# Kernel optimization log

Measured on AMD Instinct MI355X. Metric: run time of the kernel, lower is better.

## Reference

```python
import jax, jax.numpy as jnp
import numpy as np

N_NODES = 100000
N_EDGES = 1200000
D_IN = 64
D_HID = 64
D_OUT = 64


def setup_inputs() -> dict:
    key = jax.random.key(0)
    k1, k2, k3, k4, k5, k6 = jax.random.split(key, 6)
    x = jax.random.normal(k1, (N_NODES, D_IN), dtype=jnp.float32)
    edge_index = jax.random.randint(k2, (2, N_EDGES), 0, N_NODES, dtype=jnp.int32)
    s1 = 1.0 / np.sqrt(2 * D_IN)
    s2 = 1.0 / np.sqrt(2 * D_HID)
    W1 = jax.random.uniform(k3, (2 * D_IN, D_HID), jnp.float32, -s1, s1)
    b1 = jax.random.uniform(k4, (D_HID,), jnp.float32, -s1, s1)
    W2 = jax.random.uniform(k5, (2 * D_HID, D_OUT), jnp.float32, -s2, s2)
    b2 = jax.random.uniform(k6, (D_OUT,), jnp.float32, -s2, s2)
    return {"x": x, "edge_index": edge_index, "W1": W1, "b1": b1, "W2": W2, "b2": b2}


def _sage_conv(x, row, col, W, b):
    n = x.shape[0]
    # gather neighbor features and scatter-sum to destinations
    neighbor_sum = jax.ops.segment_sum(x[col], row, num_segments=n)  # [N, d]
    deg = jax.ops.segment_sum(jnp.ones(row.shape[0], x.dtype), row, num_segments=n)
    deg = jnp.maximum(deg, 1.0)
    neighbor_agg = neighbor_sum / deg[:, None]
    out = jnp.concatenate([x, neighbor_agg], axis=-1)  # [N, 2d]
    return out @ W + b


def reference(x, edge_index, W1, b1, W2, b2):
    row, col = edge_index[0], edge_index[1]
    h = jax.nn.relu(_sage_conv(x, row, col, W1, b1))
    # dropout is identity at inference (training=False)
    return _sage_conv(h, row, col, W2, b2)
```

## Files before the change

### kernel.cpp

```cpp
#include <hip/hip_runtime.h>

#define N_NODES 100000
#define N_EDGES 1200000
#define D 64

#define BSHIFT 8
#define NB ((N_NODES + 255) >> BSHIFT)
#define EPB 2048
#define P1_BLOCKS ((N_EDGES + EPB - 1) / EPB)
#define P2_CAP 4096

typedef short bf16x8 __attribute__((ext_vector_type(8)));
typedef float f32x4 __attribute__((ext_vector_type(4)));
typedef unsigned short u16x4 __attribute__((ext_vector_type(4)));
typedef unsigned short u16x8 __attribute__((ext_vector_type(8)));

__device__ __forceinline__ short f2bf(float x) {
  unsigned u = __float_as_uint(x);
  unsigned r = (u + 0x7FFFu + ((u >> 16) & 1u)) >> 16;
  return (short)r;
}
__device__ __forceinline__ float bf2f(short b) {
  return __uint_as_float(((unsigned)(unsigned short)b) << 16);
}

__device__ __forceinline__ void w_swz(const float* __restrict__ W,
                                      short* __restrict__ wh,
                                      short* __restrict__ wl, int blk) {
  int i = blk * 256 + threadIdx.x;
  int j = i & 7;
  int l = (i >> 3) & 63;
  int s = (i >> 9) & 3;
  int t = i >> 11;
  int k = s * 32 + ((l >> 4) * 8) + j;
  int n = t * 16 + (l & 15);
  float v = W[k * 64 + n];
  short hb = f2bf(v);
  wh[i] = hb;
  wl[i] = f2bf(v - bf2f(hb));
}

__global__ __launch_bounds__(256) void prep(
    const float* __restrict__ x, unsigned short* __restrict__ xh,
    unsigned short* __restrict__ xl,
    const float* __restrict__ W1, short* __restrict__ w1h, short* __restrict__ w1l,
    const float* __restrict__ W2, short* __restrict__ w2h, short* __restrict__ w2l) {
  const int bid = blockIdx.x;
  if (bid < 32) { w_swz(W1, w1h, w1l, bid); return; }
  if (bid < 64) { w_swz(W2, w2h, w2l, bid - 32); return; }
  int i = (bid - 64) * 256 + threadIdx.x;
  if (i >= N_NODES * D / 8) return;
  const float4 a0 = *(const float4*)(x + (size_t)i * 8);
  const float4 a1 = *(const float4*)(x + (size_t)i * 8 + 4);
  const float f[8] = {a0.x, a0.y, a0.z, a0.w, a1.x, a1.y, a1.z, a1.w};
  u16x8 vh, vl;
#pragma unroll
  for (int j = 0; j < 8; ++j) {
    const short hb = f2bf(f[j]);
    vh[j] = (unsigned short)hb;
    vl[j] = (unsigned short)f2bf(f[j] - bf2f(hb));
  }
  *(u16x8*)(xh + (size_t)i * 8) = vh;
  *(u16x8*)(xl + (size_t)i * 8) = vl;
}

__global__ __launch_bounds__(256) void p1_count(const int* __restrict__ row,
                                                int* __restrict__ bucketCount) {
  __shared__ int h[NB];
  const int t = threadIdx.x;
  for (int i = t; i < NB; i += 256) h[i] = 0;
  __syncthreads();
  const int base = blockIdx.x * EPB;
#pragma unroll
  for (int i = 0; i < EPB / 256; ++i) {
    int e = base + i * 256 + t;
    if (e < N_EDGES) atomicAdd(&h[row[e] >> BSHIFT], 1);
  }
  __syncthreads();
  for (int i = t; i < NB; i += 256)
    if (h[i]) atomicAdd(&bucketCount[i], h[i]);
}

__global__ __launch_bounds__(512) void p1_scan(const int* __restrict__ bucketCount,
                                               int* __restrict__ bucketStart,
                                               int* __restrict__ cursor) {
  __shared__ int lds[512];
  const int t = threadIdx.x;
  int v = (t < NB) ? bucketCount[t] : 0;
  lds[t] = v;
  __syncthreads();
  for (int off = 1; off < 512; off <<= 1) {
    int add = (t >= off) ? lds[t - off] : 0;
    __syncthreads();
    lds[t] += add;
    __syncthreads();
  }
  if (t < NB) {
    int start = lds[t] - v;
    bucketStart[t] = start;
    cursor[t] = start;
  }
  if (t == NB - 1) bucketStart[NB] = lds[t];
}

__global__ __launch_bounds__(512) void p1_scatter(
    const int* __restrict__ row, const int* __restrict__ col,
    int* __restrict__ cursor, unsigned long long* __restrict__ pairBuf) {
  __shared__ int h[NB];
  __shared__ int hexcl[NB];
  __shared__ int gbase[NB];
  __shared__ int scan_lds[512];
  __shared__ unsigned long long staged[EPB];
  const int t = threadIdx.x;
  for (int i = t; i < NB; i += 512) h[i] = 0;
  __syncthreads();
  const int base = blockIdx.x * EPB;
  const int cnt = min(EPB, N_EDGES - base);

  int myrank[EPB / 512];
  int mybkt[EPB / 512];
  unsigned long long mypair[EPB / 512];
#pragma unroll
  for (int i = 0; i < EPB / 512; ++i) {
    int e = base + i * 512 + t;
    if (e < N_EDGES) {
      unsigned r = (unsigned)row[e];
      unsigned c = (unsigned)col[e];
      int b = (int)(r >> BSHIFT);
      mybkt[i] = b;
      mypair[i] = ((unsigned long long)r << 32) | c;
      myrank[i] = atomicAdd(&h[b], 1);
    } else {
      mybkt[i] = -1;
    }
  }
  __syncthreads();
  int v = (t < NB) ? h[t] : 0;
  scan_lds[t] = v;
  __syncthreads();
  for (int off = 1; off < 512; off <<= 1) {
    int add = (t >= off) ? scan_lds[t - off] : 0;
    __syncthreads();
    scan_lds[t] += add;
    __syncthreads();
  }
  if (t < NB) {
    hexcl[t] = scan_lds[t] - v;
    gbase[t] = (h[t] > 0) ? atomicAdd(&cursor[t], h[t]) : 0;
  }
  __syncthreads();
#pragma unroll
  for (int i = 0; i < EPB / 512; ++i)
    if (mybkt[i] >= 0) staged[hexcl[mybkt[i]] + myrank[i]] = mypair[i];
  __syncthreads();
  for (int i = t; i < cnt; i += 512) {
    unsigned long long p = staged[i];
    int b = (int)(p >> (32 + BSHIFT));
    pairBuf[gbase[b] + (i - hexcl[b])] = p;
  }
}

__global__ __launch_bounds__(256) void p2_csr(
    const unsigned long long* __restrict__ pairBuf,
    const int* __restrict__ bucketStart,
    int* __restrict__ ends, int* __restrict__ sortedCol) {
  __shared__ int hist[256];
  __shared__ int sc[256];
  __shared__ unsigned short rankLDS[P2_CAP];
  const int t = threadIdx.x;
  const int b = blockIdx.x;
  const int base = bucketStart[b];
  const int cnt = min(bucketStart[b + 1] - base, P2_CAP);
  hist[t] = 0;
  __syncthreads();
  for (int i = t; i < cnt; i += 256) {
    int lr = (int)((pairBuf[base + i] >> 32) & ((1 << BSHIFT) - 1));
    rankLDS[i] = (unsigned short)atomicAdd(&hist[lr], 1);
  }
  __syncthreads();
  int v = hist[t];
  sc[t] = v;
  __syncthreads();
  for (int off = 1; off < 256; off <<= 1) {
    int add = (t >= off) ? sc[t - off] : 0;
    __syncthreads();
    sc[t] += add;
    __syncthreads();
  }
  const int node = (b << BSHIFT) + t;
  if (node < N_NODES) ends[node] = base + sc[t];
  const int excl = sc[t] - v;
  __syncthreads();
  sc[t] = excl;
  __syncthreads();
  for (int i = t; i < cnt; i += 256) {
    unsigned long long p = pairBuf[base + i];
    int lr = (int)((p >> 32) & ((1 << BSHIFT) - 1));
    sortedCol[base + sc[lr] + (int)rankLDS[i]] = (int)(unsigned)p;
  }
}

__global__ __launch_bounds__(256) void sage_agg(
    const unsigned short* __restrict__ xb, const int* __restrict__ ends,
    const int* __restrict__ sortedCol, unsigned short* __restrict__ agg, int n) {
  const int lane = threadIdx.x & 63;
  const int g = lane >> 4;
  const int fq = lane & 15;
  const int gwave = (blockIdx.x * blockDim.x + threadIdx.x) >> 6;
  const int nwaves = (gridDim.x * blockDim.x) >> 6;

  for (int r = gwave; r < n; r += nwaves) {
    const int start = (r == 0) ? 0 : ends[r - 1];
    const int end = ends[r];
    const int deg = end - start;
    float4 acc = make_float4(0.f, 0.f, 0.f, 0.f);

    for (int base = start; base < end; base += 64) {
      const int m = min(64, end - base);
      const int cv = (lane < m) ? sortedCol[base + lane] : 0;
      for (int j = 0; j < m; j += 16) {
        const int i0 = j + 0 + g, i1 = j + 4 + g, i2 = j + 8 + g, i3 = j + 12 + g;
        const int c0 = __shfl(cv, i0 < m ? i0 : 0);
        const int c1 = __shfl(cv, i1 < m ? i1 : 0);
        const int c2 = __shfl(cv, i2 < m ? i2 : 0);
        const int c3 = __shfl(cv, i3 < m ? i3 : 0);
        u16x4 v0, v1, v2, v3;
        if (i0 < m) v0 = *(const u16x4*)(xb + (size_t)c0 * D + fq * 4);
        if (i1 < m) v1 = *(const u16x4*)(xb + (size_t)c1 * D + fq * 4);
        if (i2 < m) v2 = *(const u16x4*)(xb + (size_t)c2 * D + fq * 4);
        if (i3 < m) v3 = *(const u16x4*)(xb + (size_t)c3 * D + fq * 4);
        if (i0 < m) { acc.x += bf2f(v0[0]); acc.y += bf2f(v0[1]);
                      acc.z += bf2f(v0[2]); acc.w += bf2f(v0[3]); }
        if (i1 < m) { acc.x += bf2f(v1[0]); acc.y += bf2f(v1[1]);
                      acc.z += bf2f(v1[2]); acc.w += bf2f(v1[3]); }
        if (i2 < m) { acc.x += bf2f(v2[0]); acc.y += bf2f(v2[1]);
                      acc.z += bf2f(v2[2]); acc.w += bf2f(v2[3]); }
        if (i3 < m) { acc.x += bf2f(v3[0]); acc.y += bf2f(v3[1]);
                      acc.z += bf2f(v3[2]); acc.w += bf2f(v3[3]); }
      }
    }
    acc.x += __shfl_xor(acc.x, 16); acc.x += __shfl_xor(acc.x, 32);
    acc.y += __shfl_xor(acc.y, 16); acc.y += __shfl_xor(acc.y, 32);
    acc.z += __shfl_xor(acc.z, 16); acc.z += __shfl_xor(acc.z, 32);
    acc.w += __shfl_xor(acc.w, 16); acc.w += __shfl_xor(acc.w, 32);
    if (g == 0) {
      const float s = 1.0f / (float)max(deg, 1);
      u16x4 o;
      o[0] = (unsigned short)f2bf(acc.x * s);
      o[1] = (unsigned short)f2bf(acc.y * s);
      o[2] = (unsigned short)f2bf(acc.z * s);
      o[3] = (unsigned short)f2bf(acc.w * s);
      *(u16x4*)(agg + (size_t)r * D + fq * 4) = o;
    }
  }
}

__global__ __launch_bounds__(256) void sage_mm(
    const unsigned short* __restrict__ ah, const unsigned short* __restrict__ al,
    const unsigned short* __restrict__ aggb,
    const short* __restrict__ wh, const short* __restrict__ wl,
    const float* __restrict__ b, float* __restrict__ out,
    unsigned short* __restrict__ hh, unsigned short* __restrict__ hl,
    int doRelu) {
  const int lane = threadIdx.x & 63;
  const int m = lane & 15;
  const int q = lane >> 4;
  const int gwave = (blockIdx.x * blockDim.x + threadIdx.x) >> 6;
  const int nwaves = (gridDim.x * blockDim.x) >> 6;
  const int nTiles = N_NODES / 16;

  for (int tile = gwave; tile < nTiles; tile += nwaves) {
    const int r0 = tile * 16;
    f32x4 acc[4];
#pragma unroll
    for (int t = 0; t < 4; ++t) {
      const float bv = b[t * 16 + m];
      acc[t][0] = bv; acc[t][1] = bv; acc[t][2] = bv; acc[t][3] = bv;
    }

#pragma unroll
    for (int s = 0; s < 4; ++s) {
      const int kb = (s & 1) * 32 + q * 8;
      const size_t ai = (size_t)(r0 + m) * D + kb;
      bf16x8 Ah, Al;
      if (s < 2) {
        Ah = *(const bf16x8*)(ah + ai);
        Al = *(const bf16x8*)(al + ai);
      } else {
        Ah = *(const bf16x8*)(aggb + ai);
      }
#pragma unroll
      for (int t = 0; t < 4; ++t) {
        const int bi = ((t * 4 + s) * 64 + lane) * 8;
        const bf16x8 Bh = *(const bf16x8*)(wh + bi);
        const bf16x8 Bl = *(const bf16x8*)(wl + bi);
        acc[t] = __builtin_amdgcn_mfma_f32_16x16x32_bf16(Ah, Bh, acc[t], 0, 0, 0);
        acc[t] = __builtin_amdgcn_mfma_f32_16x16x32_bf16(Ah, Bl, acc[t], 0, 0, 0);
        if (s < 2)
          acc[t] = __builtin_amdgcn_mfma_f32_16x16x32_bf16(Al, Bh, acc[t], 0, 0, 0);
      }
    }

#pragma unroll
    for (int t = 0; t < 4; ++t) {
#pragma unroll
      for (int rg = 0; rg < 4; ++rg) {
        float v = acc[t][rg];
        const size_t oi = (size_t)(r0 + q * 4 + rg) * D + t * 16 + m;
        if (doRelu) {
          v = fmaxf(v, 0.0f);
          const short hv = f2bf(v);
          hh[oi] = (unsigned short)hv;
          hl[oi] = (unsigned short)f2bf(v - bf2f(hv));
        } else {
          out[oi] = v;
        }
      }
    }
  }
}

extern "C" void kernel_launch(void* const* d_in, const int* in_sizes, int n_in,
                              void* d_out, int out_size, void* d_ws, size_t ws_size,
                              hipStream_t stream) {
  const float* x  = (const float*)d_in[0];
  const int*   ei = (const int*)d_in[1];
  const float* W1 = (const float*)d_in[2];
  const float* b1 = (const float*)d_in[3];
  const float* W2 = (const float*)d_in[4];
  const float* b2 = (const float*)d_in[5];
  float* out = (float*)d_out;

  const int* row = ei;
  const int* col = ei + N_EDGES;

  char* ws = (char*)d_ws;
  int* endsArr = (int*)ws;
  size_t off = ((size_t)N_NODES * sizeof(int) + 4095) & ~(size_t)4095;
  int* sortedCol = (int*)(ws + off);
  off += ((size_t)N_EDGES * sizeof(int) + 4095) & ~(size_t)4095;
  int* bucketCount = (int*)(ws + off);
  int* bucketStart = bucketCount + 512;
  int* cursor = bucketStart + 512;
  off += 8192;
  short* w1h = (short*)(ws + off); off += 8192 * sizeof(short);
  short* w1l = (short*)(ws + off); off += 8192 * sizeof(short);
  short* w2h = (short*)(ws + off); off += 8192 * sizeof(short);
  short* w2l = (short*)(ws + off); off += 8192 * sizeof(short);
  unsigned short* xh = (unsigned short*)(ws + off);
  off += (size_t)N_NODES * D * sizeof(unsigned short);
  unsigned short* xl = (unsigned short*)(ws + off);
  off += (size_t)N_NODES * D * sizeof(unsigned short);
  unsigned short* hh = (unsigned short*)(ws + off);
  off += (size_t)N_NODES * D * sizeof(unsigned short);
  unsigned short* hl = (unsigned short*)(ws + off);
  off += (size_t)N_NODES * D * sizeof(unsigned short);
  off = (off + 4095) & ~(size_t)4095;
  unsigned long long* pairBuf = (unsigned long long*)(ws + off);
  unsigned short* aggbf = (unsigned short*)(ws + off);

  hipMemsetAsync(bucketCount, 0, NB * sizeof(int), stream);

  prep<<<64 + (N_NODES * D / 8 + 255) / 256, 256, 0, stream>>>(
      x, xh, xl, W1, w1h, w1l, W2, w2h, w2l);

  p1_count<<<P1_BLOCKS, 256, 0, stream>>>(row, bucketCount);
  p1_scan<<<1, 512, 0, stream>>>(bucketCount, bucketStart, cursor);
  p1_scatter<<<P1_BLOCKS, 512, 0, stream>>>(row, col, cursor, pairBuf);
  p2_csr<<<NB, 256, 0, stream>>>(pairBuf, bucketStart, endsArr, sortedCol);

  sage_agg<<<2048, 256, 0, stream>>>(xh, endsArr, sortedCol, aggbf, N_NODES);
  sage_mm<<<1563, 256, 0, stream>>>(xh, xl, aggbf, w1h, w1l, b1, out, hh, hl, 1);

  sage_agg<<<2048, 256, 0, stream>>>(hh, endsArr, sortedCol, aggbf, N_NODES);
  sage_mm<<<1563, 256, 0, stream>>>(hh, hl, aggbf, w2h, w2l, b2, out, hh, hl, 0);
}
```

Baseline: 234.3 us.

## Fuse neighbor aggregation with MFMA projection and drop low-bf16 activation halves

Merges the gather-mean aggregation and the split-bf16 MFMA matmul into one kernel. Each block handles 16 nodes, stages the aggregated rows in LDS and has each wave compute one 16-column output tile. This removes the global round trip of the aggregate buffer and two launches per layer. It also folds weight/x preparation into the edge-count kernel. Activations now keep only the high bf16 half instead of a hi/lo pair, which cuts memory traffic and MFMA work but lowers accuracy of the activation operand.

```diff
diff --git a/kernel.cpp b/kernel.cpp
--- a/kernel.cpp
+++ b/kernel.cpp
@@ -9,6 +9,10 @@
 #define EPB 2048
 #define P1_BLOCKS ((N_EDGES + EPB - 1) / EPB)
 #define P2_CAP 4096
+
+#define XSPLIT_BLOCKS (N_NODES * D / 8 / 256)
+#define PREP_BLOCKS (XSPLIT_BLOCKS + 64)
+#define PC_BLOCKS (PREP_BLOCKS + P1_BLOCKS)
 
 typedef short bf16x8 __attribute__((ext_vector_type(8)));
 typedef float f32x4 __attribute__((ext_vector_type(4)));
@@ -40,37 +44,30 @@
   wl[i] = f2bf(v - bf2f(hb));
 }
 
-__global__ __launch_bounds__(256) void prep(
+__global__ __launch_bounds__(256) void prep_count(
     const float* __restrict__ x, unsigned short* __restrict__ xh,
-    unsigned short* __restrict__ xl,
     const float* __restrict__ W1, short* __restrict__ w1h, short* __restrict__ w1l,
-    const float* __restrict__ W2, short* __restrict__ w2h, short* __restrict__ w2l) {
+    const float* __restrict__ W2, short* __restrict__ w2h, short* __restrict__ w2l,
+    const int* __restrict__ row, int* __restrict__ bucketCount) {
   const int bid = blockIdx.x;
-  if (bid < 32) { w_swz(W1, w1h, w1l, bid); return; }
-  if (bid < 64) { w_swz(W2, w2h, w2l, bid - 32); return; }
-  int i = (bid - 64) * 256 + threadIdx.x;
-  if (i >= N_NODES * D / 8) return;
-  const float4 a0 = *(const float4*)(x + (size_t)i * 8);
-  const float4 a1 = *(const float4*)(x + (size_t)i * 8 + 4);
-  const float f[8] = {a0.x, a0.y, a0.z, a0.w, a1.x, a1.y, a1.z, a1.w};
-  u16x8 vh, vl;
-#pragma unroll
-  for (int j = 0; j < 8; ++j) {
-    const short hb = f2bf(f[j]);
-    vh[j] = (unsigned short)hb;
-    vl[j] = (unsigned short)f2bf(f[j] - bf2f(hb));
-  }
-  *(u16x8*)(xh + (size_t)i * 8) = vh;
-  *(u16x8*)(xl + (size_t)i * 8) = vl;
-}
-
-__global__ __launch_bounds__(256) void p1_count(const int* __restrict__ row,
-                                                int* __restrict__ bucketCount) {
+  const int t = threadIdx.x;
+  if (bid < XSPLIT_BLOCKS) {
+    int i = bid * 256 + t;
+    const float4 a0 = *(const float4*)(x + (size_t)i * 8);
+    const float4 a1 = *(const float4*)(x + (size_t)i * 8 + 4);
+    const float f[8] = {a0.x, a0.y, a0.z, a0.w, a1.x, a1.y, a1.z, a1.w};
+    u16x8 vh;
+#pragma unroll
+    for (int j = 0; j < 8; ++j) vh[j] = (unsigned short)f2bf(f[j]);
+    *(u16x8*)(xh + (size_t)i * 8) = vh;
+    return;
+  }
+  if (bid < XSPLIT_BLOCKS + 32) { w_swz(W1, w1h, w1l, bid - XSPLIT_BLOCKS); return; }
+  if (bid < PREP_BLOCKS)        { w_swz(W2, w2h, w2l, bid - XSPLIT_BLOCKS - 32); return; }
   __shared__ int h[NB];
-  const int t = threadIdx.x;
   for (int i = t; i < NB; i += 256) h[i] = 0;
   __syncthreads();
-  const int base = blockIdx.x * EPB;
+  const int base = (bid - PREP_BLOCKS) * EPB;
 #pragma unroll
   for (int i = 0; i < EPB / 256; ++i) {
     int e = base + i * 256 + t;
@@ -200,18 +197,31 @@
   }
 }
 
-__global__ __launch_bounds__(256) void sage_agg(
-    const unsigned short* __restrict__ xb, const int* __restrict__ ends,
-    const int* __restrict__ sortedCol, unsigned short* __restrict__ agg, int n) {
-  const int lane = threadIdx.x & 63;
+__global__ __launch_bounds__(256) void sage_fused(
+    const unsigned short* __restrict__ xsrc, const int* __restrict__ ends,
+    const int* __restrict__ sortedCol,
+    const short* __restrict__ wh, const short* __restrict__ wl,
+    const float* __restrict__ bias, float* __restrict__ outf,
+    unsigned short* __restrict__ outb, int doRelu) {
+  __shared__ unsigned short aggS[16][72];
+  __shared__ int ends_s[17];
+  const int tid = threadIdx.x;
+  const int w = tid >> 6;
+  const int lane = tid & 63;
   const int g = lane >> 4;
   const int fq = lane & 15;
-  const int gwave = (blockIdx.x * blockDim.x + threadIdx.x) >> 6;
-  const int nwaves = (gridDim.x * blockDim.x) >> 6;
-
-  for (int r = gwave; r < n; r += nwaves) {
-    const int start = (r == 0) ? 0 : ends[r - 1];
-    const int end = ends[r];
+  const int r0 = blockIdx.x * 16;
+
+  if (tid < 17) {
+    int idx = r0 - 1 + tid;
+    ends_s[tid] = (idx >= 0) ? ends[idx] : 0;
+  }
+  __syncthreads();
+
+  for (int i = 0; i < 4; ++i) {
+    const int rl = w * 4 + i;
+    const int start = ends_s[rl];
+    const int end = ends_s[rl + 1];
     const int deg = end - start;
     float4 acc = make_float4(0.f, 0.f, 0.f, 0.f);
 
@@ -225,10 +235,10 @@
         const int c2 = __shfl(cv, i2 < m ? i2 : 0);
         const int c3 = __shfl(cv, i3 < m ? i3 : 0);
         u16x4 v0, v1, v2, v3;
-        if (i0 < m) v0 = *(const u16x4*)(xb + (size_t)c0 * D + fq * 4);
-        if (i1 < m) v1 = *(const u16x4*)(xb + (size_t)c1 * D + fq * 4);
-        if (i2 < m) v2 = *(const u16x4*)(xb + (size_t)c2 * D + fq * 4);
-        if (i3 < m) v3 = *(const u16x4*)(xb + (size_t)c3 * D + fq * 4);
+        if (i0 < m) v0 = *(const u16x4*)(xsrc + (size_t)c0 * D + fq * 4);
+        if (i1 < m) v1 = *(const u16x4*)(xsrc + (size_t)c1 * D + fq * 4);
+        if (i2 < m) v2 = *(const u16x4*)(xsrc + (size_t)c2 * D + fq * 4);
+        if (i3 < m) v3 = *(const u16x4*)(xsrc + (size_t)c3 * D + fq * 4);
         if (i0 < m) { acc.x += bf2f(v0[0]); acc.y += bf2f(v0[1]);
                       acc.z += bf2f(v0[2]); acc.w += bf2f(v0[3]); }
         if (i1 < m) { acc.x += bf2f(v1[0]); acc.y += bf2f(v1[1]);
@@ -250,72 +260,43 @@
       o[1] = (unsigned short)f2bf(acc.y * s);
       o[2] = (unsigned short)f2bf(acc.z * s);
       o[3] = (unsigned short)f2bf(acc.w * s);
-      *(u16x4*)(agg + (size_t)r * D + fq * 4) = o;
-    }
-  }
-}
-
-__global__ __launch_bounds__(256) void sage_mm(
-    const unsigned short* __restrict__ ah, const unsigned short* __restrict__ al,
-    const unsigned short* __restrict__ aggb,
-    const short* __restrict__ wh, const short* __restrict__ wl,
-    const float* __restrict__ b, float* __restrict__ out,
-    unsigned short* __restrict__ hh, unsigned short* __restrict__ hl,
-    int doRelu) {
-  const int lane = threadIdx.x & 63;
+      *(u16x4*)(&aggS[rl][fq * 4]) = o;
+    }
+  }
+  __syncthreads();
+
   const int m = lane & 15;
   const int q = lane >> 4;
-  const int gwave = (blockIdx.x * blockDim.x + threadIdx.x) >> 6;
-  const int nwaves = (gridDim.x * blockDim.x) >> 6;
-  const int nTiles = N_NODES / 16;
-
-  for (int tile = gwave; tile < nTiles; tile += nwaves) {
-    const int r0 = tile * 16;
-    f32x4 acc[4];
-#pragma unroll
-    for (int t = 0; t < 4; ++t) {
-      const float bv = b[t * 16 + m];
-      acc[t][0] = bv; acc[t][1] = bv; acc[t][2] = bv; acc[t][3] = bv;
-    }
-
-#pragma unroll
-    for (int s = 0; s < 4; ++s) {
-      const int kb = (s & 1) * 32 + q * 8;
-      const size_t ai = (size_t)(r0 + m) * D + kb;
-      bf16x8 Ah, Al;
-      if (s < 2) {
-        Ah = *(const bf16x8*)(ah + ai);
-        Al = *(const bf16x8*)(al + ai);
-      } else {
-        Ah = *(const bf16x8*)(aggb + ai);
-      }
-#pragma unroll
-      for (int t = 0; t < 4; ++t) {
-        const int bi = ((t * 4 + s) * 64 + lane) * 8;
-        const bf16x8 Bh = *(const bf16x8*)(wh + bi);
-        const bf16x8 Bl = *(const bf16x8*)(wl + bi);
-        acc[t] = __builtin_amdgcn_mfma_f32_16x16x32_bf16(Ah, Bh, acc[t], 0, 0, 0);
-        acc[t] = __builtin_amdgcn_mfma_f32_16x16x32_bf16(Ah, Bl, acc[t], 0, 0, 0);
-        if (s < 2)
-          acc[t] = __builtin_amdgcn_mfma_f32_16x16x32_bf16(Al, Bh, acc[t], 0, 0, 0);
-      }
-    }
-
-#pragma unroll
-    for (int t = 0; t < 4; ++t) {
-#pragma unroll
-      for (int rg = 0; rg < 4; ++rg) {
-        float v = acc[t][rg];
-        const size_t oi = (size_t)(r0 + q * 4 + rg) * D + t * 16 + m;
-        if (doRelu) {
-          v = fmaxf(v, 0.0f);
-          const short hv = f2bf(v);
-          hh[oi] = (unsigned short)hv;
-          hl[oi] = (unsigned short)f2bf(v - bf2f(hv));
-        } else {
-          out[oi] = v;
-        }
-      }
+  f32x4 acc;
+  {
+    const float bv = bias[w * 16 + m];
+    acc[0] = bv; acc[1] = bv; acc[2] = bv; acc[3] = bv;
+  }
+#pragma unroll
+  for (int s = 0; s < 4; ++s) {
+    const int kb = (s & 1) * 32 + q * 8;
+    bf16x8 Ah;
+    if (s < 2) {
+      Ah = *(const bf16x8*)(xsrc + (size_t)(r0 + m) * D + kb);
+    } else {
+      Ah = *(const bf16x8*)(&aggS[m][kb]);
+    }
+    const int bi = ((w * 4 + s) * 64 + lane) * 8;
+    const bf16x8 Bh = *(const bf16x8*)(wh + bi);
+    const bf16x8 Bl = *(const bf16x8*)(wl + bi);
+    acc = __builtin_amdgcn_mfma_f32_16x16x32_bf16(Ah, Bh, acc, 0, 0, 0);
+    acc = __builtin_amdgcn_mfma_f32_16x16x32_bf16(Ah, Bl, acc, 0, 0, 0);
+  }
+
+#pragma unroll
+  for (int rg = 0; rg < 4; ++rg) {
+    float v = acc[rg];
+    const size_t oi = (size_t)(r0 + q * 4 + rg) * D + w * 16 + m;
+    if (doRelu) {
+      v = fmaxf(v, 0.0f);
+      outb[oi] = (unsigned short)f2bf(v);
+    } else {
+      outf[oi] = v;
     }
   }
 }
@@ -349,29 +330,23 @@
   short* w2l = (short*)(ws + off); off += 8192 * sizeof(short);
   unsigned short* xh = (unsigned short*)(ws + off);
   off += (size_t)N_NODES * D * sizeof(unsigned short);
-  unsigned short* xl = (unsigned short*)(ws + off);
-  off += (size_t)N_NODES * D * sizeof(unsigned short);
   unsigned short* hh = (unsigned short*)(ws + off);
-  off += (size_t)N_NODES * D * sizeof(unsigned short);
-  unsigned short* hl = (unsigned short*)(ws + off);
   off += (size_t)N_NODES * D * sizeof(unsigned short);
   off = (off + 4095) & ~(size_t)4095;
   unsigned long long* pairBuf = (unsigned long long*)(ws + off);
-  unsigned short* aggbf = (unsigned short*)(ws + off);
 
   hipMemsetAsync(bucketCount, 0, NB * sizeof(int), stream);
 
-  prep<<<64 + (N_NODES * D / 8 + 255) / 256, 256, 0, stream>>>(
-      x, xh, xl, W1, w1h, w1l, W2, w2h, w2l);
-
-  p1_count<<<P1_BLOCKS, 256, 0, stream>>>(row, bucketCount);
+  prep_count<<<PC_BLOCKS, 256, 0, stream>>>(x, xh, W1, w1h, w1l, W2, w2h, w2l,
+                                            row, bucketCount);
+
   p1_scan<<<1, 512, 0, stream>>>(bucketCount, bucketStart, cursor);
   p1_scatter<<<P1_BLOCKS, 512, 0, stream>>>(row, col, cursor, pairBuf);
   p2_csr<<<NB, 256, 0, stream>>>(pairBuf, bucketStart, endsArr, sortedCol);
 
-  sage_agg<<<2048, 256, 0, stream>>>(xh, endsArr, sortedCol, aggbf, N_NODES);
-  sage_mm<<<1563, 256, 0, stream>>>(xh, xl, aggbf, w1h, w1l, b1, out, hh, hl, 1);
-
-  sage_agg<<<2048, 256, 0, stream>>>(hh, endsArr, sortedCol, aggbf, N_NODES);
-  sage_mm<<<1563, 256, 0, stream>>>(hh, hl, aggbf, w2h, w2l, b2, out, hh, hl, 0);
-}
+  sage_fused<<<N_NODES / 16, 256, 0, stream>>>(xh, endsArr, sortedCol,
+                                               w1h, w1l, b1, out, hh, 1);
+
+  sage_fused<<<N_NODES / 16, 256, 0, stream>>>(hh, endsArr, sortedCol,
+                                               w2h, w2l, b2, out, hh, 0);
+}
```

Result: faster. 213.9 us (-8.7%).
